# Kernel tuning notes

Hardware: AMD Instinct MI355X
Metric: run time of the kernel (lower is better)

The kernel has to match this reference:

```python
import jax, jax.numpy as jnp
import numpy as np

P, N, K, F = 4, 4096, 2, 256
E = 8            # num_experts
H = 4 * 256      # ffn_ratio * output_dim
OUT = 256        # output_dim


def setup_inputs() -> dict:
    key = jax.random.key(0)
    ks = jax.random.split(key, 9)
    s = 0.02
    return {
        "x_parts": jax.random.normal(ks[0], (P, N, K, F), dtype=jnp.float32),
        "selected_experts": jax.random.randint(ks[1], (P, N, K), 0, E, dtype=jnp.int64),
        # SwiGLU: gate and up projections F -> H (per expert)
        "Wg": jax.random.normal(ks[2], (E, F, H), dtype=jnp.float32) * s,
        "bg": jnp.zeros((E, H), dtype=jnp.float32),
        "Wu": jax.random.normal(ks[3], (E, F, H), dtype=jnp.float32) * s,
        "bu": jnp.zeros((E, H), dtype=jnp.float32),
        # man_fc (Euclidean): Linear(H,H) -> ReLU -> Linear(H,OUT)
        "W1": jax.random.normal(ks[4], (E, H, H), dtype=jnp.float32) * s,
        "b1": jnp.zeros((E, H), dtype=jnp.float32),
        "W2": jax.random.normal(ks[5], (E, H, OUT), dtype=jnp.float32) * s,
        "b2": jnp.zeros((E, OUT), dtype=jnp.float32),
    }


def _expert(x, Wg, bg, Wu, bu, W1, b1, W2, b2):
    # x: [T, F] -> [T, OUT]; SwiGLU then Linear-ReLU-Linear (Euclidean man_fc)
    h = jax.nn.silu(x @ Wg + bg) * (x @ Wu + bu)   # [T, H]
    h = jax.nn.relu(h @ W1 + b1)                    # [T, H]
    return h @ W2 + b2                              # [T, OUT]


def reference(x_parts, selected_experts, Wg, bg, Wu, bu, W1, b1, W2, b2):
    # Each (p, i, k) token-copy is processed by expert selected_experts[p,i,k];
    # dense masked combine replaces the Python-level gather/scatter loops.
    x = x_parts.reshape(-1, F)                      # [T, F], T = P*N*K
    sel = selected_experts.reshape(-1)              # [T]
    out = jnp.zeros((x.shape[0], OUT), dtype=x_parts.dtype)
    for e in range(E):
        y = _expert(x, Wg[e], bg[e], Wu[e], bu[e], W1[e], b1[e], W2[e], b2[e])
        out = out + jnp.where((sel == e)[:, None], y, 0.0)
    return out.reshape(P, N, K, OUT)
```

## Files before the change

kernel.cpp:

```cpp
#include <hip/hip_runtime.h>
#include <hip/hip_bf16.h>
#include <cstdint>
#include <cstddef>

#define NTOK 32768
#define FD   256
#define HD   1024
#define OD   256
#define NEXP 8

#define BM 128
#define BN 128
#define BK 32
#define MAX_TILES 272

typedef __bf16 bf16;
typedef __bf16 bf16x8 __attribute__((ext_vector_type(8)));
typedef __bf16 bf16x4 __attribute__((ext_vector_type(4)));
typedef float  f32x4  __attribute__((ext_vector_type(4)));

__device__ __forceinline__ void cp16(const void* g, void* l) {
    __builtin_amdgcn_global_load_lds(
        (const __attribute__((address_space(1))) void*)g,
        (__attribute__((address_space(3))) void*)l, 16, 0, 0);
}

static const size_t O_CNT  = 0;
static const size_t O_CUR  = 64;
static const size_t O_OFF  = 128;
static const size_t O_NT   = 192;
static const size_t O_TE   = 1024;
static const size_t O_TR   = 3072;
static const size_t O_PERM = 5120;
static const size_t O_XP   = 136192;
static const size_t O_WG   = 16913408;
static const size_t O_WU   = 21107712;
static const size_t O_W1   = 25302016;
static const size_t O_W2   = 42079232;
static const size_t O_H    = 46273536;
static const size_t O_H2   = 113382400;

__global__ void k_hist(const int* __restrict__ sel, int* __restrict__ cnt) {
    __shared__ int lcnt[NEXP];
    if (threadIdx.x < NEXP) lcnt[threadIdx.x] = 0;
    __syncthreads();
    int t = blockIdx.x * 256 + threadIdx.x;
    atomicAdd(&lcnt[sel[t]], 1);
    __syncthreads();
    if (threadIdx.x < NEXP) atomicAdd(&cnt[threadIdx.x], lcnt[threadIdx.x]);
}

__global__ void k_plan(const int* __restrict__ cnt, int* __restrict__ off,
                       int* __restrict__ tileE, int* __restrict__ tileR,
                       int* __restrict__ nt) {
    if (threadIdx.x == 0 && blockIdx.x == 0) {
        int o = 0;
        for (int e = 0; e < NEXP; e++) { off[e] = o; o += cnt[e]; }
        off[NEXP] = o;
        int n = 0;
        for (int e = 0; e < NEXP; e++) {
            int c = cnt[e];
            int nte = (c + BM - 1) / BM;
            for (int r = 0; r < nte; r++) { tileE[n] = e; tileR[n] = r; n++; }
        }
        *nt = n;
    }
}

__global__ void k_scatter(const int* __restrict__ sel, const int* __restrict__ off,
                          int* __restrict__ cur, int* __restrict__ perm) {
    __shared__ int lcnt[NEXP];
    __shared__ int lbase[NEXP];
    if (threadIdx.x < NEXP) lcnt[threadIdx.x] = 0;
    __syncthreads();
    int t = blockIdx.x * 256 + threadIdx.x;
    int e = sel[t];
    int rank = atomicAdd(&lcnt[e], 1);
    __syncthreads();
    if (threadIdx.x < NEXP)
        lbase[threadIdx.x] = atomicAdd(&cur[threadIdx.x], lcnt[threadIdx.x]);
    __syncthreads();
    perm[off[e] + lbase[e] + rank] = t;
}

__global__ void k_gather(const float* __restrict__ x, const int* __restrict__ perm,
                         bf16* __restrict__ Xp) {
    int gid = blockIdx.x * 256 + threadIdx.x;
    int pos = gid >> 6;
    int c   = gid & 63;
    int tok = perm[pos];
    float4 v = ((const float4*)x)[(size_t)tok * 64 + c];
    bf16x4 o;
    o.x = (bf16)v.x; o.y = (bf16)v.y; o.z = (bf16)v.z; o.w = (bf16)v.w;
    *(bf16x4*)&Xp[(size_t)pos * FD + c * 4] = o;
}

#define TPE 448
__global__ void k_transpose_all(const float* __restrict__ Wg, bf16* __restrict__ Wgt,
                                const float* __restrict__ Wu, bf16* __restrict__ Wut,
                                const float* __restrict__ W1, bf16* __restrict__ W1t,
                                const float* __restrict__ W2, bf16* __restrict__ W2t) {
    __shared__ float tile[64][65];
    int b  = blockIdx.x;
    int e  = b / TPE;
    int tt = b % TPE;
    const float* Ws; bf16* Wd; int K, N;
    if (tt < 64)       { Ws = Wg; Wd = Wgt; K = FD; N = HD; }
    else if (tt < 128) { Ws = Wu; Wd = Wut; K = FD; N = HD; tt -= 64; }
    else if (tt < 384) { Ws = W1; Wd = W1t; K = HD; N = HD; tt -= 128; }
    else               { Ws = W2; Wd = W2t; K = HD; N = OD; tt -= 384; }
    int nk = K / 64;
    int k0 = (tt % nk) * 64, n0 = (tt / nk) * 64;
    Ws += (size_t)e * K * N;
    Wd += (size_t)e * K * N;
    int t = threadIdx.x;
    for (int q = 0; q < 4; q++) {
        int lin = t + q * 256;
        int r = lin >> 4, c4 = (lin & 15) * 4;
        float4 v = *(const float4*)&Ws[(size_t)(k0 + r) * N + n0 + c4];
        tile[r][c4] = v.x; tile[r][c4+1] = v.y; tile[r][c4+2] = v.z; tile[r][c4+3] = v.w;
    }
    __syncthreads();
    for (int q = 0; q < 2; q++) {
        int lin = t + q * 256;
        int n = lin >> 3, k8 = (lin & 7) * 8;
        bf16x8 o;
        for (int i = 0; i < 8; i++) o[i] = (bf16)tile[k8 + i][n];
        *(bf16x8*)&Wd[(size_t)(n0 + n) * K + k0 + k8] = o;
    }
}


#define GEMM_PROLOGUE(KDIM)                                                    \
    if (blockIdx.x >= *ntp) return;                                            \
    __shared__ bf16 As[BM * BK];                                               \
    __shared__ bf16 Bs[BN * BK];                                               \
    int e    = tileE[blockIdx.x];                                              \
    int row0 = tileR[blockIdx.x] * BM;                                         \
    int base = off[e];                                                         \
    int valid = off[e + 1] - base - row0; if (valid > BM) valid = BM;          \
    int n0 = blockIdx.y * BN;                                                  \
    int tid = threadIdx.x;                                                     \
    int lane = tid & 63, wv = tid >> 6;                                        \
    int wm = wv & 1, wn = wv >> 1;                                             \
    int lr = lane & 15, qd = lane >> 4;                                        \
    f32x4 acc[4][4] = {};

#define GEMM_KLOOP(KDIM)                                                       \
    for (int k0 = 0; k0 < (KDIM); k0 += BK) {                                  \
        for (int s = 0; s < 2; s++) {                                          \
            int ci = tid + s * 256;                                            \
            int m  = ci >> 2;                                                  \
            int jg = (ci & 3) ^ ((m >> 1) & 3);                                \
            int mc = m < valid ? m : valid - 1;                                \
            cp16(Ab + (size_t)mc * (KDIM) + k0 + jg * 8, &As[ci * 8]);         \
            cp16(Bb + (size_t)m  * (KDIM) + k0 + jg * 8, &Bs[ci * 8]);         \
        }                                                                      \
        __syncthreads();                                                       \
        bf16x8 af[4], bfr[4];                                                  \
        for (int i = 0; i < 4; i++) {                                          \
            int row = wm * 64 + i * 16 + lr;                                   \
            int sl  = qd ^ ((row >> 1) & 3);                                   \
            af[i] = *(const bf16x8*)&As[row * BK + sl * 8];                    \
        }                                                                      \
        for (int j = 0; j < 4; j++) {                                          \
            int row = wn * 64 + j * 16 + lr;                                   \
            int sl  = qd ^ ((row >> 1) & 3);                                   \
            bfr[j] = *(const bf16x8*)&Bs[row * BK + sl * 8];                   \
        }                                                                      \
        for (int i = 0; i < 4; i++)                                            \
            for (int j = 0; j < 4; j++)                                        \
                acc[i][j] = __builtin_amdgcn_mfma_f32_16x16x32_bf16(           \
                    af[i], bfr[j], acc[i][j], 0, 0, 0);                        \
        __syncthreads();                                                       \
    }

__global__ __launch_bounds__(256, 4) void k_swiglu(
    const bf16* __restrict__ Xp, const bf16* __restrict__ Wgt, const bf16* __restrict__ Wut,
    const float* __restrict__ bg, const float* __restrict__ bu, bf16* __restrict__ Hbuf,
    const int* __restrict__ tileE, const int* __restrict__ tileR,
    const int* __restrict__ off, const int* __restrict__ ntp)
{
    if (blockIdx.x >= *ntp) return;
    __shared__ bf16 As [BM * BK];
    __shared__ bf16 Bgs[64 * BK];
    __shared__ bf16 Bus[64 * BK];
    int e    = tileE[blockIdx.x];
    int row0 = tileR[blockIdx.x] * BM;
    int base = off[e];
    int valid = off[e + 1] - base - row0; if (valid > BM) valid = BM;
    int n0 = blockIdx.y * 64;
    int tid = threadIdx.x;
    int lane = tid & 63, wv = tid >> 6;
    int wm = wv & 1, wn = wv >> 1;
    int lr = lane & 15, qd = lane >> 4;

    f32x4 accg[4][2] = {};
    f32x4 accu[4][2] = {};
    const bf16* Ab  = Xp  + (size_t)(base + row0) * FD;
    const bf16* Bgb = Wgt + ((size_t)e * HD + n0) * FD;
    const bf16* Bub = Wut + ((size_t)e * HD + n0) * FD;

    for (int k0 = 0; k0 < FD; k0 += BK) {
        for (int s = 0; s < 2; s++) {
            int ci = tid + s * 256;
            int m  = ci >> 2;
            int jg = (ci & 3) ^ ((m >> 1) & 3);
            int mc = m < valid ? m : valid - 1;
            cp16(Ab + (size_t)mc * FD + k0 + jg * 8, &As[ci * 8]);
        }
        {
            int ci = tid;
            int m  = ci >> 2;
            int jg = (ci & 3) ^ ((m >> 1) & 3);
            cp16(Bgb + (size_t)m * FD + k0 + jg * 8, &Bgs[ci * 8]);
            cp16(Bub + (size_t)m * FD + k0 + jg * 8, &Bus[ci * 8]);
        }
        __syncthreads();
        bf16x8 af[4], bgf[2], buf[2];
        for (int i = 0; i < 4; i++) {
            int row = wm * 64 + i * 16 + lr;
            int sl  = qd ^ ((row >> 1) & 3);
            af[i] = *(const bf16x8*)&As[row * BK + sl * 8];
        }
        for (int j = 0; j < 2; j++) {
            int row = wn * 32 + j * 16 + lr;
            int sl  = qd ^ ((row >> 1) & 3);
            bgf[j] = *(const bf16x8*)&Bgs[row * BK + sl * 8];
            buf[j] = *(const bf16x8*)&Bus[row * BK + sl * 8];
        }
        for (int i = 0; i < 4; i++)
            for (int j = 0; j < 2; j++) {
                accg[i][j] = __builtin_amdgcn_mfma_f32_16x16x32_bf16(af[i], bgf[j], accg[i][j], 0, 0, 0);
                accu[i][j] = __builtin_amdgcn_mfma_f32_16x16x32_bf16(af[i], buf[j], accu[i][j], 0, 0, 0);
            }
        __syncthreads();
    }
    for (int i = 0; i < 4; i++) {
        int rb = wm * 64 + i * 16 + qd * 4;
        for (int r = 0; r < 4; r++) {
            int m = rb + r;
            if (m >= valid) continue;
            size_t orow = (size_t)(base + row0 + m) * HD;
            for (int j = 0; j < 2; j++) {
                int n = n0 + wn * 32 + j * 16 + lr;
                float g = accg[i][j][r] + bg[e * HD + n];
                float u = accu[i][j][r] + bu[e * HD + n];
                float h = g * u / (1.f + __expf(-g));
                Hbuf[orow + n] = (bf16)h;
            }
        }
    }
}

__global__ __launch_bounds__(256, 4) void k_gemm2(
    const bf16* __restrict__ Ain, const bf16* __restrict__ Bt, const float* __restrict__ bias,
    bf16* __restrict__ Out,
    const int* __restrict__ tileE, const int* __restrict__ tileR,
    const int* __restrict__ off, const int* __restrict__ ntp)
{
    GEMM_PROLOGUE(HD)
    const bf16* Ab = Ain + (size_t)(base + row0) * HD;
    const bf16* Bb = Bt  + ((size_t)e * HD + n0) * HD;
    GEMM_KLOOP(HD)
    for (int i = 0; i < 4; i++) {
        int rb = wm * 64 + i * 16 + qd * 4;
        for (int r = 0; r < 4; r++) {
            int m = rb + r;
            if (m >= valid) continue;
            size_t orow = (size_t)(base + row0 + m) * HD;
            for (int j = 0; j < 4; j++) {
                int n = n0 + wn * 64 + j * 16 + lr;
                float v = acc[i][j][r] + bias[e * HD + n];
                Out[orow + n] = (bf16)(v > 0.f ? v : 0.f);
            }
        }
    }
}

__global__ __launch_bounds__(256, 4) void k_gemm3(
    const bf16* __restrict__ Ain, const bf16* __restrict__ Bt, const float* __restrict__ bias,
    float* __restrict__ out, const int* __restrict__ perm,
    const int* __restrict__ tileE, const int* __restrict__ tileR,
    const int* __restrict__ off, const int* __restrict__ ntp)
{
    GEMM_PROLOGUE(HD)
    const bf16* Ab = Ain + (size_t)(base + row0) * HD;
    const bf16* Bb = Bt  + ((size_t)e * OD + n0) * HD;
    GEMM_KLOOP(HD)
    for (int i = 0; i < 4; i++) {
        int rb = wm * 64 + i * 16 + qd * 4;
        for (int r = 0; r < 4; r++) {
            int m = rb + r;
            if (m >= valid) continue;
            int tok = perm[base + row0 + m];
            size_t orow = (size_t)tok * OD;
            for (int j = 0; j < 4; j++) {
                int n = n0 + wn * 64 + j * 16 + lr;
                out[orow + n] = acc[i][j][r] + bias[e * OD + n];
            }
        }
    }
}

extern "C" void kernel_launch(void* const* d_in, const int* in_sizes, int n_in,
                              void* d_out, int out_size, void* d_ws, size_t ws_size,
                              hipStream_t stream) {
    const float* x   = (const float*)d_in[0];
    const int*   sel = (const int*)d_in[1];
    const float* Wg  = (const float*)d_in[2];
    const float* bg  = (const float*)d_in[3];
    const float* Wu  = (const float*)d_in[4];
    const float* bu  = (const float*)d_in[5];
    const float* W1  = (const float*)d_in[6];
    const float* b1  = (const float*)d_in[7];
    const float* W2  = (const float*)d_in[8];
    const float* b2  = (const float*)d_in[9];
    float* out = (float*)d_out;

    char* ws = (char*)d_ws;
    int* cnt   = (int*)(ws + O_CNT);
    int* cur   = (int*)(ws + O_CUR);
    int* off   = (int*)(ws + O_OFF);
    int* nt    = (int*)(ws + O_NT);
    int* tileE = (int*)(ws + O_TE);
    int* tileR = (int*)(ws + O_TR);
    int* perm  = (int*)(ws + O_PERM);
    bf16* Xp   = (bf16*)(ws + O_XP);
    bf16* Wgt  = (bf16*)(ws + O_WG);
    bf16* Wut  = (bf16*)(ws + O_WU);
    bf16* W1t  = (bf16*)(ws + O_W1);
    bf16* W2t  = (bf16*)(ws + O_W2);
    bf16* Hbuf = (bf16*)(ws + O_H);
    bf16* H2   = (bf16*)(ws + O_H2);

    hipMemsetAsync(ws, 0, 256, stream);

    k_hist   <<<NTOK / 256, 256, 0, stream>>>(sel, cnt);
    k_plan   <<<1, 64, 0, stream>>>(cnt, off, tileE, tileR, nt);
    k_scatter<<<NTOK / 256, 256, 0, stream>>>(sel, off, cur, perm);
    k_gather <<<NTOK * 64 / 256, 256, 0, stream>>>(x, perm, Xp);

    k_transpose_all<<<NEXP * TPE, 256, 0, stream>>>(Wg, Wgt, Wu, Wut, W1, W1t, W2, W2t);

    k_swiglu<<<dim3(MAX_TILES, HD / 64), 256, 0, stream>>>(Xp, Wgt, Wut, bg, bu, Hbuf,
                                                           tileE, tileR, off, nt);
    k_gemm2 <<<dim3(MAX_TILES, HD / BN), 256, 0, stream>>>(Hbuf, W1t, b1, H2,
                                                           tileE, tileR, off, nt);
    k_gemm3 <<<dim3(MAX_TILES, OD / BN), 256, 0, stream>>>(H2, W2t, b2, out, perm,
                                                           tileE, tileR, off, nt);
}
```

Measured before the change: 364.4 us.

## Double BK to 64 and remap grid so row tiles stay on one XCD

```diff
diff --git a/kernel.cpp b/kernel.cpp
--- a/kernel.cpp
+++ b/kernel.cpp
@@ -11,8 +11,9 @@
 
 #define BM 128
 #define BN 128
-#define BK 32
-#define MAX_TILES 272
+#define BK 64
+#define MAXRT 34
+#define RT8 34
 
 typedef __bf16 bf16;
 typedef __bf16 bf16x8 __attribute__((ext_vector_type(8)));
@@ -131,69 +132,63 @@
 }
 
 
-#define GEMM_PROLOGUE(KDIM)                                                    \
-    if (blockIdx.x >= *ntp) return;                                            \
-    __shared__ bf16 As[BM * BK];                                               \
-    __shared__ bf16 Bs[BN * BK];                                               \
-    int e    = tileE[blockIdx.x];                                              \
-    int row0 = tileR[blockIdx.x] * BM;                                         \
+#define DECODE_TILE(NTY, BNE)                                                  \
+    int L = blockIdx.x;                                                        \
+    int xcd = L & 7; int tq = L >> 3;                                          \
+    int ny  = tq % (NTY); int Rhi = tq / (NTY);                                \
+    int R   = Rhi * 8 + xcd;                                                   \
+    if (R >= *ntp) return;                                                     \
+    int e    = tileE[R];                                                       \
+    int row0 = tileR[R] * BM;                                                  \
     int base = off[e];                                                         \
     int valid = off[e + 1] - base - row0; if (valid > BM) valid = BM;          \
-    int n0 = blockIdx.y * BN;                                                  \
+    int n0 = ny * (BNE);                                                       \
     int tid = threadIdx.x;                                                     \
     int lane = tid & 63, wv = tid >> 6;                                        \
     int wm = wv & 1, wn = wv >> 1;                                             \
-    int lr = lane & 15, qd = lane >> 4;                                        \
-    f32x4 acc[4][4] = {};
+    int lr = lane & 15, qd = lane >> 4;
 
 #define GEMM_KLOOP(KDIM)                                                       \
     for (int k0 = 0; k0 < (KDIM); k0 += BK) {                                  \
-        for (int s = 0; s < 2; s++) {                                          \
+        for (int s = 0; s < 4; s++) {                                          \
             int ci = tid + s * 256;                                            \
-            int m  = ci >> 2;                                                  \
-            int jg = (ci & 3) ^ ((m >> 1) & 3);                                \
-            int mc = m < valid ? m : valid - 1;                                \
-            cp16(Ab + (size_t)mc * (KDIM) + k0 + jg * 8, &As[ci * 8]);         \
-            cp16(Bb + (size_t)m  * (KDIM) + k0 + jg * 8, &Bs[ci * 8]);         \
+            int row = ci >> 3;                                                 \
+            int jg  = (ci & 7) ^ (row & 7);                                    \
+            int mc  = row < valid ? row : valid - 1;                           \
+            cp16(Ab + (size_t)mc  * (KDIM) + k0 + jg * 8, &As[ci * 8]);        \
+            cp16(Bb + (size_t)row * (KDIM) + k0 + jg * 8, &Bs[ci * 8]);        \
         }                                                                      \
         __syncthreads();                                                       \
-        bf16x8 af[4], bfr[4];                                                  \
-        for (int i = 0; i < 4; i++) {                                          \
-            int row = wm * 64 + i * 16 + lr;                                   \
-            int sl  = qd ^ ((row >> 1) & 3);                                   \
-            af[i] = *(const bf16x8*)&As[row * BK + sl * 8];                    \
+        for (int ks = 0; ks < 2; ks++) {                                       \
+            bf16x8 af[4], bfr[4];                                              \
+            for (int i = 0; i < 4; i++) {                                      \
+                int row = wm * 64 + i * 16 + lr;                               \
+                int sl  = (ks * 4 + qd) ^ (row & 7);                           \
+                af[i] = *(const bf16x8*)&As[row * BK + sl * 8];                \
+            }                                                                  \
+            for (int j = 0; j < 4; j++) {                                      \
+                int row = wn * 64 + j * 16 + lr;                               \
+                int sl  = (ks * 4 + qd) ^ (row & 7);                           \
+                bfr[j] = *(const bf16x8*)&Bs[row * BK + sl * 8];               \
+            }                                                                  \
+            for (int i = 0; i < 4; i++)                                        \
+                for (int j = 0; j < 4; j++)                                    \
+                    acc[i][j] = __builtin_amdgcn_mfma_f32_16x16x32_bf16(       \
+                        af[i], bfr[j], acc[i][j], 0, 0, 0);                    \
         }                                                                      \
-        for (int j = 0; j < 4; j++) {                                          \
-            int row = wn * 64 + j * 16 + lr;                                   \
-            int sl  = qd ^ ((row >> 1) & 3);                                   \
-            bfr[j] = *(const bf16x8*)&Bs[row * BK + sl * 8];                   \
-        }                                                                      \
-        for (int i = 0; i < 4; i++)                                            \
-            for (int j = 0; j < 4; j++)                                        \
-                acc[i][j] = __builtin_amdgcn_mfma_f32_16x16x32_bf16(           \
-                    af[i], bfr[j], acc[i][j], 0, 0, 0);                        \
         __syncthreads();                                                       \
     }
 
-__global__ __launch_bounds__(256, 4) void k_swiglu(
+__global__ __launch_bounds__(256, 3) void k_swiglu(
     const bf16* __restrict__ Xp, const bf16* __restrict__ Wgt, const bf16* __restrict__ Wut,
     const float* __restrict__ bg, const float* __restrict__ bu, bf16* __restrict__ Hbuf,
     const int* __restrict__ tileE, const int* __restrict__ tileR,
     const int* __restrict__ off, const int* __restrict__ ntp)
 {
-    if (blockIdx.x >= *ntp) return;
     __shared__ bf16 As [BM * BK];
     __shared__ bf16 Bgs[64 * BK];
     __shared__ bf16 Bus[64 * BK];
-    int e    = tileE[blockIdx.x];
-    int row0 = tileR[blockIdx.x] * BM;
-    int base = off[e];
-    int valid = off[e + 1] - base - row0; if (valid > BM) valid = BM;
-    int n0 = blockIdx.y * 64;
-    int tid = threadIdx.x;
-    int lane = tid & 63, wv = tid >> 6;
-    int wm = wv & 1, wn = wv >> 1;
-    int lr = lane & 15, qd = lane >> 4;
+    DECODE_TILE(16, 64)
 
     f32x4 accg[4][2] = {};
     f32x4 accu[4][2] = {};
@@ -202,38 +197,40 @@
     const bf16* Bub = Wut + ((size_t)e * HD + n0) * FD;
 
     for (int k0 = 0; k0 < FD; k0 += BK) {
+        for (int s = 0; s < 4; s++) {
+            int ci = tid + s * 256;
+            int row = ci >> 3;
+            int jg  = (ci & 7) ^ (row & 7);
+            int mc  = row < valid ? row : valid - 1;
+            cp16(Ab + (size_t)mc * FD + k0 + jg * 8, &As[ci * 8]);
+        }
         for (int s = 0; s < 2; s++) {
             int ci = tid + s * 256;
-            int m  = ci >> 2;
-            int jg = (ci & 3) ^ ((m >> 1) & 3);
-            int mc = m < valid ? m : valid - 1;
-            cp16(Ab + (size_t)mc * FD + k0 + jg * 8, &As[ci * 8]);
-        }
-        {
-            int ci = tid;
-            int m  = ci >> 2;
-            int jg = (ci & 3) ^ ((m >> 1) & 3);
-            cp16(Bgb + (size_t)m * FD + k0 + jg * 8, &Bgs[ci * 8]);
-            cp16(Bub + (size_t)m * FD + k0 + jg * 8, &Bus[ci * 8]);
+            int row = ci >> 3;
+            int jg  = (ci & 7) ^ (row & 7);
+            cp16(Bgb + (size_t)row * FD + k0 + jg * 8, &Bgs[ci * 8]);
+            cp16(Bub + (size_t)row * FD + k0 + jg * 8, &Bus[ci * 8]);
         }
         __syncthreads();
-        bf16x8 af[4], bgf[2], buf[2];
-        for (int i = 0; i < 4; i++) {
-            int row = wm * 64 + i * 16 + lr;
-            int sl  = qd ^ ((row >> 1) & 3);
-            af[i] = *(const bf16x8*)&As[row * BK + sl * 8];
-        }
-        for (int j = 0; j < 2; j++) {
-            int row = wn * 32 + j * 16 + lr;
-            int sl  = qd ^ ((row >> 1) & 3);
-            bgf[j] = *(const bf16x8*)&Bgs[row * BK + sl * 8];
-            buf[j] = *(const bf16x8*)&Bus[row * BK + sl * 8];
-        }
-        for (int i = 0; i < 4; i++)
+        for (int ks = 0; ks < 2; ks++) {
+            bf16x8 af[4], bgf[2], buf[2];
+            for (int i = 0; i < 4; i++) {
+                int row = wm * 64 + i * 16 + lr;
+                int sl  = (ks * 4 + qd) ^ (row & 7);
+                af[i] = *(const bf16x8*)&As[row * BK + sl * 8];
+            }
             for (int j = 0; j < 2; j++) {
-                accg[i][j] = __builtin_amdgcn_mfma_f32_16x16x32_bf16(af[i], bgf[j], accg[i][j], 0, 0, 0);
-                accu[i][j] = __builtin_amdgcn_mfma_f32_16x16x32_bf16(af[i], buf[j], accu[i][j], 0, 0, 0);
-            }
+                int row = wn * 32 + j * 16 + lr;
+                int sl  = (ks * 4 + qd) ^ (row & 7);
+                bgf[j] = *(const bf16x8*)&Bgs[row * BK + sl * 8];
+                buf[j] = *(const bf16x8*)&Bus[row * BK + sl * 8];
+            }
+            for (int i = 0; i < 4; i++)
+                for (int j = 0; j < 2; j++) {
+                    accg[i][j] = __builtin_amdgcn_mfma_f32_16x16x32_bf16(af[i], bgf[j], accg[i][j], 0, 0, 0);
+                    accu[i][j] = __builtin_amdgcn_mfma_f32_16x16x32_bf16(af[i], buf[j], accu[i][j], 0, 0, 0);
+                }
+        }
         __syncthreads();
     }
     for (int i = 0; i < 4; i++) {
@@ -253,13 +250,16 @@
     }
 }
 
-__global__ __launch_bounds__(256, 4) void k_gemm2(
+__global__ __launch_bounds__(256, 3) void k_gemm2(
     const bf16* __restrict__ Ain, const bf16* __restrict__ Bt, const float* __restrict__ bias,
     bf16* __restrict__ Out,
     const int* __restrict__ tileE, const int* __restrict__ tileR,
     const int* __restrict__ off, const int* __restrict__ ntp)
 {
-    GEMM_PROLOGUE(HD)
+    __shared__ bf16 As[BM * BK];
+    __shared__ bf16 Bs[BN * BK];
+    DECODE_TILE(8, BN)
+    f32x4 acc[4][4] = {};
     const bf16* Ab = Ain + (size_t)(base + row0) * HD;
     const bf16* Bb = Bt  + ((size_t)e * HD + n0) * HD;
     GEMM_KLOOP(HD)
@@ -278,13 +278,16 @@
     }
 }
 
-__global__ __launch_bounds__(256, 4) void k_gemm3(
+__global__ __launch_bounds__(256, 3) void k_gemm3(
     const bf16* __restrict__ Ain, const bf16* __restrict__ Bt, const float* __restrict__ bias,
     float* __restrict__ out, const int* __restrict__ perm,
     const int* __restrict__ tileE, const int* __restrict__ tileR,
     const int* __restrict__ off, const int* __restrict__ ntp)
 {
-    GEMM_PROLOGUE(HD)
+    __shared__ bf16 As[BM * BK];
+    __shared__ bf16 Bs[BN * BK];
+    DECODE_TILE(2, BN)
+    f32x4 acc[4][4] = {};
     const bf16* Ab = Ain + (size_t)(base + row0) * HD;
     const bf16* Bb = Bt  + ((size_t)e * OD + n0) * HD;
     GEMM_KLOOP(HD)
@@ -343,10 +346,10 @@
 
     k_transpose_all<<<NEXP * TPE, 256, 0, stream>>>(Wg, Wgt, Wu, Wut, W1, W1t, W2, W2t);
 
-    k_swiglu<<<dim3(MAX_TILES, HD / 64), 256, 0, stream>>>(Xp, Wgt, Wut, bg, bu, Hbuf,
-                                                           tileE, tileR, off, nt);
-    k_gemm2 <<<dim3(MAX_TILES, HD / BN), 256, 0, stream>>>(Hbuf, W1t, b1, H2,
-                                                           tileE, tileR, off, nt);
-    k_gemm3 <<<dim3(MAX_TILES, OD / BN), 256, 0, stream>>>(H2, W2t, b2, out, perm,
-                                                           tileE, tileR, off, nt);
-}
+    k_swiglu<<<RT8 * 16 * 8, 256, 0, stream>>>(Xp, Wgt, Wut, bg, bu, Hbuf,
+                                               tileE, tileR, off, nt);
+    k_gemm2 <<<RT8 * 8 * 8, 256, 0, stream>>>(Hbuf, W1t, b1, H2,
+                                              tileE, tileR, off, nt);
+    k_gemm3 <<<RT8 * 2 * 8, 256, 0, stream>>>(H2, W2t, b2, out, perm,
+                                              tileE, tileR, off, nt);
+}
```

Measured after the change: 340.6 us. 6.5% less time.
